# Kernel tuning notes

Measured on AMD Instinct MI355X. Metric: run time of the kernel, lower is better.

The kernel has to match this reference:

```python
import jax, jax.numpy as jnp
import numpy as np
import math

B, C, L = 16, 256, 8192
D_INNER, ATT_DIM = 512, 64


def setup_inputs() -> dict:
    key = jax.random.key(0)
    k1, k2, k3, k4, k5 = jax.random.split(key, 5)
    # Linear(1, att_dim) weights are [att_dim, 1]; store squeezed as [att_dim].
    # Match nn.Linear default init: U(-1, 1) since fan_in = 1.
    lim_rank1 = 1.0
    lim_out = 1.0 / math.sqrt(ATT_DIM)
    return {
        "h_v": jax.random.normal(k1, (B, C, L), dtype=jnp.float32),
        "wq": jax.random.uniform(k2, (ATT_DIM,), jnp.float32, -lim_rank1, lim_rank1),
        "wk": jax.random.uniform(k3, (ATT_DIM,), jnp.float32, -lim_rank1, lim_rank1),
        "wv": jax.random.uniform(k4, (ATT_DIM,), jnp.float32, -lim_rank1, lim_rank1),
        "w_out": jax.random.uniform(k5, (D_INNER, ATT_DIM), jnp.float32, -lim_out, lim_out),
    }


def reference(h_v, wq, wk, wv, w_out):
    # h_v: [B, C, L]
    att_dim = wq.shape[0]
    scale = 1.0 / math.sqrt(att_dim)
    # q = (mean_c h_v) * wq, k = h_v * wk  (rank-1 projections of Linear(1, att_dim)),
    # so (q * k).sum(-1) = h_v * mean_c(h_v) * <wq, wk> without materializing [B,C,L,att].
    s = jnp.mean(h_v, axis=1, keepdims=True)          # [B, 1, L]
    qk = jnp.dot(wq, wk)                              # scalar <wq, wk>
    logits = h_v * s * (qk * scale)                   # [B, C, L]
    alpha = jax.nn.softmax(logits, axis=1)            # softmax over channel axis C
    # psi_latent = sum_c alpha * (h_v[...,None] * wv) = (sum_c alpha*h_v) outer wv
    pooled = jnp.sum(alpha * h_v, axis=1)             # [B, L]
    psi_latent = pooled[..., None] * wv               # [B, L, att_dim]
    psi = jnp.einsum("bla,da->bdl", psi_latent, w_out)  # [B, d_inner, L]
    return psi
```

## Files before the change

kernel.cpp:

```cpp
#include <hip/hip_runtime.h>

#define B_DIM 16
#define C_DIM 256
#define L_DIM 8192
#define D_INNER 512
#define ATT 64


__global__ __launch_bounds__(512) void prep_kernel(
    const float* __restrict__ wq, const float* __restrict__ wk,
    const float* __restrict__ wv, const float* __restrict__ w_out,
    float* __restrict__ ws) {
    int d = threadIdx.x;
    float acc = 0.f;
    #pragma unroll
    for (int a = 0; a < ATT; ++a) acc += w_out[d * ATT + a] * wv[a];
    ws[64 + d] = acc;
    if (d == 0) {
        float qk = 0.f;
        #pragma unroll
        for (int a = 0; a < ATT; ++a) qk += wq[a] * wk[a];
        ws[0] = qk * 0.125f;
    }
}

__global__ __launch_bounds__(256) void pooled_kernel(
    const float* __restrict__ h_v, const float* __restrict__ ws,
    float* __restrict__ pooled) {
    const float t_scale = ws[0];
    int tid = blockIdx.x * blockDim.x + threadIdx.x;
    int b  = tid >> 12;
    int l2 = tid & 4095;
    const float2* src = (const float2*)(h_v + (size_t)b * C_DIM * L_DIM) + l2;

    float s0 = 0.f, s1 = 0.f;
    float mn0 = __builtin_inff(), mn1 = __builtin_inff();
    float mx0 = -__builtin_inff(), mx1 = -__builtin_inff();
    #pragma unroll 8
    for (int c = 0; c < C_DIM; ++c) {
        float2 v = src[(size_t)c * (L_DIM / 2)];
        s0 += v.x; s1 += v.y;
        mn0 = fminf(mn0, v.x); mx0 = fmaxf(mx0, v.x);
        mn1 = fminf(mn1, v.y); mx1 = fmaxf(mx1, v.y);
    }
    float t0 = s0 * (1.0f / C_DIM) * t_scale;
    float t1 = s1 * (1.0f / C_DIM) * t_scale;
    float m0 = fmaxf(mn0 * t0, mx0 * t0);
    float m1 = fmaxf(mn1 * t1, mx1 * t1);

    float se0 = 0.f, se1 = 0.f, sp0 = 0.f, sp1 = 0.f;
    #pragma unroll 8
    for (int c = 0; c < C_DIM; ++c) {
        float2 v = src[(size_t)c * (L_DIM / 2)];
        float e0 = __expf(v.x * t0 - m0);
        float e1 = __expf(v.y * t1 - m1);
        se0 += e0; se1 += e1;
        sp0 += e0 * v.x; sp1 += e1 * v.y;
    }
    float2 o;
    o.x = sp0 / se0;
    o.y = sp1 / se1;
    ((float2*)pooled)[tid] = o;
}

__global__ __launch_bounds__(256) void write_kernel(
    const float* __restrict__ ws, float* __restrict__ out) {
    const float* wo_v   = ws + 64;
    const float* pooled = ws + 1024;
    int i   = blockIdx.x * 256 + threadIdx.x;
    int l4  = i & 2047;
    int tmp = i >> 11;
    int d   = tmp & 511;
    int b   = tmp >> 9;
    float4 p = ((const float4*)(pooled + (size_t)b * L_DIM))[l4];
    float  w = wo_v[d];
    float4 o;
    o.x = p.x * w; o.y = p.y * w; o.z = p.z * w; o.w = p.w * w;
    ((float4*)out)[i] = o;
}

extern "C" void kernel_launch(void* const* d_in, const int* in_sizes, int n_in,
                              void* d_out, int out_size, void* d_ws, size_t ws_size,
                              hipStream_t stream) {
    const float* h_v   = (const float*)d_in[0];
    const float* wq    = (const float*)d_in[1];
    const float* wk    = (const float*)d_in[2];
    const float* wv    = (const float*)d_in[3];
    const float* w_out = (const float*)d_in[4];
    float* ws  = (float*)d_ws;
    float* out = (float*)d_out;

    hipLaunchKernelGGL(prep_kernel, dim3(1), dim3(512), 0, stream,
                       wq, wk, wv, w_out, ws);
    hipLaunchKernelGGL(pooled_kernel, dim3(256), dim3(256), 0, stream,
                       h_v, ws, ws + 1024);
    hipLaunchKernelGGL(write_kernel, dim3(65536), dim3(256), 0, stream,
                       ws, out);
}
```

Before: 392.9 us.

## Fuse pooled softmax and output write into one tiled kernel with channel split

Result: slower. 418.9 us (+6.6%).

```diff
diff --git a/kernel.cpp b/kernel.cpp
--- a/kernel.cpp
+++ b/kernel.cpp
@@ -1,10 +1,12 @@
 #include <hip/hip_runtime.h>
+#include <math.h>
 
 #define B_DIM 16
 #define C_DIM 256
 #define L_DIM 8192
 #define D_INNER 512
 #define ATT 64
+#define TL 128
 
 
 __global__ __launch_bounds__(512) void prep_kernel(
@@ -24,59 +26,99 @@
     }
 }
 
-__global__ __launch_bounds__(256) void pooled_kernel(
+__global__ __launch_bounds__(256) void fused_kernel(
     const float* __restrict__ h_v, const float* __restrict__ ws,
-    float* __restrict__ pooled) {
+    float* __restrict__ out) {
+    __shared__ float2 red_a[4][64];
+    __shared__ float2 red_b[4][64];
+    __shared__ float2 red_c[4][64];
+    __shared__ float  pool_l[TL];
+    __shared__ float  s_wov[D_INNER];
+
+    const int t    = threadIdx.x;
+    const int cg   = t >> 6;
+    const int lane = t & 63;
+    const int b    = blockIdx.x >> 6;
+    const int lt   = blockIdx.x & 63;
+    const int l0   = lt * TL;
+
+    s_wov[t]       = ws[64 + t];
+    s_wov[t + 256] = ws[64 + t + 256];
     const float t_scale = ws[0];
-    int tid = blockIdx.x * blockDim.x + threadIdx.x;
-    int b  = tid >> 12;
-    int l2 = tid & 4095;
-    const float2* src = (const float2*)(h_v + (size_t)b * C_DIM * L_DIM) + l2;
 
-    float s0 = 0.f, s1 = 0.f;
-    float mn0 = __builtin_inff(), mn1 = __builtin_inff();
-    float mx0 = -__builtin_inff(), mx1 = -__builtin_inff();
+    const float* src = h_v + (size_t)b * (C_DIM * L_DIM) + l0 + lane * 2;
+    const int c0 = cg * 64;
+
+    float2 s  = make_float2(0.f, 0.f);
+    float2 mn = make_float2(INFINITY, INFINITY);
+    float2 mx = make_float2(-INFINITY, -INFINITY);
     #pragma unroll 8
-    for (int c = 0; c < C_DIM; ++c) {
-        float2 v = src[(size_t)c * (L_DIM / 2)];
-        s0 += v.x; s1 += v.y;
-        mn0 = fminf(mn0, v.x); mx0 = fmaxf(mx0, v.x);
-        mn1 = fminf(mn1, v.y); mx1 = fmaxf(mx1, v.y);
+    for (int c = 0; c < 64; ++c) {
+        float2 v = *(const float2*)(src + (size_t)(c0 + c) * L_DIM);
+        s.x += v.x; s.y += v.y;
+        mn.x = fminf(mn.x, v.x); mx.x = fmaxf(mx.x, v.x);
+        mn.y = fminf(mn.y, v.y); mx.y = fmaxf(mx.y, v.y);
     }
-    float t0 = s0 * (1.0f / C_DIM) * t_scale;
-    float t1 = s1 * (1.0f / C_DIM) * t_scale;
-    float m0 = fmaxf(mn0 * t0, mx0 * t0);
-    float m1 = fmaxf(mn1 * t1, mx1 * t1);
+    red_a[cg][lane] = s;
+    red_b[cg][lane] = mn;
+    red_c[cg][lane] = mx;
+    __syncthreads();
 
-    float se0 = 0.f, se1 = 0.f, sp0 = 0.f, sp1 = 0.f;
+    float2 ts  = red_a[0][lane];
+    float2 tmn = red_b[0][lane];
+    float2 tmx = red_c[0][lane];
+    #pragma unroll
+    for (int g = 1; g < 4; ++g) {
+        float2 a = red_a[g][lane], n = red_b[g][lane], x = red_c[g][lane];
+        ts.x += a.x; ts.y += a.y;
+        tmn.x = fminf(tmn.x, n.x); tmn.y = fminf(tmn.y, n.y);
+        tmx.x = fmaxf(tmx.x, x.x); tmx.y = fmaxf(tmx.y, x.y);
+    }
+    __syncthreads();
+
+    const float t0 = ts.x * (1.0f / C_DIM) * t_scale;
+    const float t1 = ts.y * (1.0f / C_DIM) * t_scale;
+    const float m0 = fmaxf(tmn.x * t0, tmx.x * t0);
+    const float m1 = fmaxf(tmn.y * t1, tmx.y * t1);
+
+    float2 se = make_float2(0.f, 0.f);
+    float2 sp = make_float2(0.f, 0.f);
     #pragma unroll 8
-    for (int c = 0; c < C_DIM; ++c) {
-        float2 v = src[(size_t)c * (L_DIM / 2)];
+    for (int c = 0; c < 64; ++c) {
+        float2 v = *(const float2*)(src + (size_t)(c0 + c) * L_DIM);
         float e0 = __expf(v.x * t0 - m0);
         float e1 = __expf(v.y * t1 - m1);
-        se0 += e0; se1 += e1;
-        sp0 += e0 * v.x; sp1 += e1 * v.y;
+        se.x += e0; se.y += e1;
+        sp.x += e0 * v.x; sp.y += e1 * v.y;
     }
-    float2 o;
-    o.x = sp0 / se0;
-    o.y = sp1 / se1;
-    ((float2*)pooled)[tid] = o;
-}
+    red_a[cg][lane] = se;
+    red_b[cg][lane] = sp;
+    __syncthreads();
 
-__global__ __launch_bounds__(256) void write_kernel(
-    const float* __restrict__ ws, float* __restrict__ out) {
-    const float* wo_v   = ws + 64;
-    const float* pooled = ws + 1024;
-    int i   = blockIdx.x * 256 + threadIdx.x;
-    int l4  = i & 2047;
-    int tmp = i >> 11;
-    int d   = tmp & 511;
-    int b   = tmp >> 9;
-    float4 p = ((const float4*)(pooled + (size_t)b * L_DIM))[l4];
-    float  w = wo_v[d];
-    float4 o;
-    o.x = p.x * w; o.y = p.y * w; o.z = p.z * w; o.w = p.w * w;
-    ((float4*)out)[i] = o;
+    float2 tse = red_a[0][lane];
+    float2 tsp = red_b[0][lane];
+    #pragma unroll
+    for (int g = 1; g < 4; ++g) {
+        float2 a = red_a[g][lane], p = red_b[g][lane];
+        tse.x += a.x; tse.y += a.y;
+        tsp.x += p.x; tsp.y += p.y;
+    }
+    if (cg == 0) {
+        ((float2*)pool_l)[lane] = make_float2(tsp.x / tse.x, tsp.y / tse.y);
+    }
+    __syncthreads();
+
+    const int dg = t >> 5;
+    const int lq = t & 31;
+    float4 pv = ((const float4*)pool_l)[lq];
+    float* ob = out + (size_t)b * ((size_t)D_INNER * L_DIM) + l0 + lq * 4;
+    #pragma unroll 8
+    for (int d = dg; d < D_INNER; d += 8) {
+        float w = s_wov[d];
+        float4 o;
+        o.x = pv.x * w; o.y = pv.y * w; o.z = pv.z * w; o.w = pv.w * w;
+        *(float4*)(ob + (size_t)d * L_DIM) = o;
+    }
 }
 
 extern "C" void kernel_launch(void* const* d_in, const int* in_sizes, int n_in,
@@ -92,8 +134,6 @@
 
     hipLaunchKernelGGL(prep_kernel, dim3(1), dim3(512), 0, stream,
                        wq, wk, wv, w_out, ws);
-    hipLaunchKernelGGL(pooled_kernel, dim3(256), dim3(256), 0, stream,
-                       h_v, ws, ws + 1024);
-    hipLaunchKernelGGL(write_kernel, dim3(65536), dim3(256), 0, stream,
-                       ws, out);
+    hipLaunchKernelGGL(fused_kernel, dim3(1024), dim3(256), 0, stream,
+                       h_v, ws, out);
 }
```
